# Performance work log

Measured on AMD Instinct MI355X. Metric: run time of the kernel, lower is better.

The kernel has to match this reference:

```python
import jax, jax.numpy as jnp
import numpy as np
from jax import lax

S = 8  # down/up-sample factor


def _seg_means(x, z):
    """Directional running means between zero-boundaries along the last axis.

    x: float [..., L] values; z: bool [..., L], True at zero-boundary positions.
    For position t strictly between consecutive boundaries (prev, nxt):
      lr[t] = mean(x[prev:t+1]),  rl[t] = mean(x[t:nxt+1]); else keep x[t].
    """
    L = x.shape[-1]
    ar = jnp.arange(L)
    ax = x.ndim - 1
    # last zero index strictly before t (-1 if none)
    idx = jnp.where(z, ar, -1)
    prev = lax.cummax(idx, axis=ax)
    prev = jnp.concatenate(
        [jnp.full(prev.shape[:-1] + (1,), -1, prev.dtype), prev[..., :-1]], axis=-1)
    # first zero index strictly after t (L if none)
    idx2 = jnp.where(z, ar, L)
    nxt = lax.cummin(idx2, axis=ax, reverse=True)
    nxt = jnp.concatenate(
        [nxt[..., 1:], jnp.full(nxt.shape[:-1] + (1,), L, nxt.dtype)], axis=-1)
    valid = (~z) & (prev >= 0) & (nxt < L)
    # padded cumsum: cs0[..., k] = sum(x[..., :k]), length L+1
    cs0 = jnp.concatenate(
        [jnp.zeros(x.shape[:-1] + (1,), x.dtype), jnp.cumsum(x, axis=-1)], axis=-1)
    prev_c = jnp.clip(prev, 0, L - 1)
    nxt_c = jnp.clip(nxt, 0, L - 1)
    sum_lr = cs0[..., 1:] - jnp.take_along_axis(cs0, prev_c, axis=-1)   # x[prev..t]
    sum_rl = jnp.take_along_axis(cs0, nxt_c + 1, axis=-1) - cs0[..., :-1]  # x[t..nxt]
    cnt_lr = jnp.maximum(ar - prev + 1, 1).astype(x.dtype)
    cnt_rl = jnp.maximum(nxt - ar + 1, 1).astype(x.dtype)
    lr = jnp.where(valid, sum_lr / cnt_lr, x)
    rl = jnp.where(valid, sum_rl / cnt_rl, x)
    return lr, rl


def setup_inputs() -> dict:
    key = jax.random.key(0)
    k0, k1 = jax.random.split(key)
    N, C, H, W = 8, 1, 2048, 2048
    x0 = jax.random.normal(k0, (N, C, H, W), dtype=jnp.float32)
    x1 = jax.random.randint(k1, (N, C, H, W), 0, 8, dtype=jnp.int32)
    return {"x0": x0, "x1": x1}


def reference(x0, x1):
    # nearest-neighbor downsample by 8 (matches F.interpolate scale_factor=1/8, mode='nearest')
    x0d = x0[..., ::S, ::S]
    zd = (x1[..., ::S, ::S] == 0)
    # horizontal pass (along rows)
    xh_lr, xh_rl = _seg_means(x0d, zd)
    # vertical pass (along columns) via transpose
    xv_tb, xv_bt = _seg_means(jnp.swapaxes(x0d, -1, -2), jnp.swapaxes(zd, -1, -2))
    y = xh_lr + xh_rl + jnp.swapaxes(xv_tb, -1, -2) + jnp.swapaxes(xv_bt, -1, -2)
    # nearest-neighbor upsample by 8
    y = jnp.repeat(jnp.repeat(y, S, axis=-2), S, axis=-1)
    return y
```

## Files before the change

kernel.cpp:

```cpp
#include <hip/hip_runtime.h>

#define DS   256
#define FULL 2048
#define NIMG 8
#define CG   4

typedef float f32x4 __attribute__((ext_vector_type(4)));
typedef int   i32x4 __attribute__((ext_vector_type(4)));

__device__ __forceinline__ float seg_fast(float x, bool z, int j,
                                          float* s_cs,
                                          unsigned long long* s_msk,
                                          float* s_ws) {
    const int lane = j & 63;
    const int w    = j >> 6;
    unsigned long long m = __ballot(z);

    float s = x;
    #pragma unroll
    for (int off = 1; off < 64; off <<= 1) {
        float t = __shfl_up(s, off, 64);
        if (lane >= off) s += t;
    }
    if (lane == 63) s_ws[w]  = s;
    if (lane == 0)  s_msk[w] = m;
    __syncthreads();

    float pre = 0.f;
    for (int ww = 0; ww < w; ++ww) pre += s_ws[ww];
    s += pre;
    s_cs[j] = s;

    unsigned long long lo = m & ((1ULL << lane) - 1ULL);
    int prev = -1;
    if (lo) prev = (w << 6) + 63 - __builtin_clzll(lo);
    else {
        for (int ww = w - 1; ww >= 0; --ww) {
            unsigned long long mm = s_msk[ww];
            if (mm) { prev = (ww << 6) + 63 - __builtin_clzll(mm); break; }
        }
    }
    unsigned long long hi = m & ~((2ULL << lane) - 1ULL);
    int nxt = DS;
    if (hi) nxt = (w << 6) + __builtin_ctzll(hi);
    else {
        for (int ww = w + 1; ww < 4; ++ww) {
            unsigned long long mm = s_msk[ww];
            if (mm) { nxt = (ww << 6) + __builtin_ctzll(mm); break; }
        }
    }
    __syncthreads();

    bool valid = (!z) && (prev >= 0) && (nxt < DS);
    if (valid) {
        float cs_j   = s_cs[j];
        float cs_pm1 = (prev > 0) ? s_cs[prev - 1] : 0.f;
        float cs_n   = s_cs[nxt];
        float cs_jm1 = (j > 0) ? s_cs[j - 1] : 0.f;
        return (cs_j - cs_pm1) / (float)(j - prev + 1)
             + (cs_n - cs_jm1) / (float)(nxt - j + 1);
    }
    return 2.f * x;
}

__global__ __launch_bounds__(256) void k_row(const float* __restrict__ x0,
                                             const int* __restrict__ x1,
                                             float2* __restrict__ xz,
                                             float* __restrict__ yH) {
    __shared__ float s_cs[DS];
    __shared__ unsigned long long s_msk[4];
    __shared__ float s_ws[4];
    const int j = threadIdx.x;
    const int line = blockIdx.x;
    const int n = line >> 8, i = line & 255;

    const float* rb0 = x0 + (size_t)(n * FULL + i * 8) * FULL;
    const int*   rb1 = x1 + (size_t)(n * FULL + i * 8) * FULL;
    f32x4 a = __builtin_nontemporal_load((const f32x4*)(rb0 + 8 * (size_t)j));
    i32x4 b = __builtin_nontemporal_load((const i32x4*)(rb1 + 8 * (size_t)j));
    float x = a[0];
    bool  z = (b[0] == 0);

    float r = seg_fast(x, z, j, s_cs, s_msk, s_ws);

    yH[(line << 8) + j] = r;
    xz[(line << 8) + j] = make_float2(x, z ? 1.f : 0.f);
}

__global__ __launch_bounds__(256) void k_colup(const float2* __restrict__ xz,
                                               const float* __restrict__ yH,
                                               f32x4* __restrict__ out) {
    __shared__ float s_x[CG][DS];
    __shared__ float s_z[CG][DS];
    __shared__ float s_out[CG][DS + 1];
    __shared__ float s_cs[DS];
    __shared__ unsigned long long s_msk[4];
    __shared__ float s_ws[4];
    const int t = threadIdx.x;
    const int g = blockIdx.x;
    const int n  = g >> 7;
    const int q  = (g >> 6) & 1;
    const int c0 = (g & 63) * CG;

    const float2* base = xz + (n << 16) + (t << 8) + c0;
    f32x4 v0 = *(const f32x4*)(base);
    f32x4 v1 = *(const f32x4*)(base + 2);
    f32x4 h  = *(const f32x4*)(yH + (n << 16) + (t << 8) + c0);
    s_x[0][t] = v0[0]; s_z[0][t] = v0[1];
    s_x[1][t] = v0[2]; s_z[1][t] = v0[3];
    s_x[2][t] = v1[0]; s_z[2][t] = v1[1];
    s_x[3][t] = v1[2]; s_z[3][t] = v1[3];

    #pragma unroll
    for (int c = 0; c < CG; ++c) {
        float x = s_x[c][t];
        bool  z = (s_z[c][t] != 0.f);
        float r = seg_fast(x, z, t, s_cs, s_msk, s_ws);
        s_out[c][t] = r + h[c];
    }
    __syncthreads();

    f32x4* ob = out + ((size_t)n << 20) + (c0 << 1);
    #pragma unroll 4
    for (int k = 0; k < 16; ++k) {
        int idx = (k << 8) + t;
        int I   = (q << 10) + (idx >> 2);
        int c   = idx & 3;
        float v = s_out[c][I >> 3];
        f32x4 vv = { v, v, v, v };
        size_t o = (size_t)I * 512 + (c << 1);
        ob[o]     = vv;
        ob[o + 1] = vv;
    }
}

extern "C" void kernel_launch(void* const* d_in, const int* in_sizes, int n_in,
                              void* d_out, int out_size, void* d_ws, size_t ws_size,
                              hipStream_t stream) {
    const float* x0 = (const float*)d_in[0];
    const int*   x1 = (const int*)d_in[1];
    f32x4* out = (f32x4*)d_out;

    float2* xz = (float2*)d_ws;
    float*  yH = (float*)(xz + NIMG * DS * DS);

    dim3 blk(256);
    k_row  <<<dim3(NIMG * DS),          blk, 0, stream>>>(x0, x1, xz, yH);
    k_colup<<<dim3(2 * NIMG * DS / CG), blk, 0, stream>>>(xz, yH, out);
}
```

Measured before the change: 43.46 us.

## Widen column-group tile to eight columns and quarter output rows per block

The column/upsample kernel now processes eight downsampled columns per block instead of four, and splits the output rows into four quarters instead of two. Each upsampled row segment written per block becomes twice as wide, so output stores are more contiguous. Column inputs now stay in registers instead of going through shared-memory staging. In exchange, each column's segment scan is recomputed by four blocks instead of two, and each block runs eight sync-heavy scans in sequence.

```diff
diff --git a/kernel.cpp b/kernel.cpp
--- a/kernel.cpp
+++ b/kernel.cpp
@@ -3,7 +3,7 @@
 #define DS   256
 #define FULL 2048
 #define NIMG 8
-#define CG   4
+#define CG   8
 
 typedef float f32x4 __attribute__((ext_vector_type(4)));
 typedef int   i32x4 __attribute__((ext_vector_type(4)));
@@ -90,8 +90,6 @@
 __global__ __launch_bounds__(256) void k_colup(const float2* __restrict__ xz,
                                                const float* __restrict__ yH,
                                                f32x4* __restrict__ out) {
-    __shared__ float s_x[CG][DS];
-    __shared__ float s_z[CG][DS];
     __shared__ float s_out[CG][DS + 1];
     __shared__ float s_cs[DS];
     __shared__ unsigned long long s_msk[4];
@@ -99,36 +97,38 @@
     const int t = threadIdx.x;
     const int g = blockIdx.x;
     const int n  = g >> 7;
-    const int q  = (g >> 6) & 1;
-    const int c0 = (g & 63) * CG;
+    const int q  = (g >> 5) & 3;
+    const int c0 = (g & 31) << 3;
 
     const float2* base = xz + (n << 16) + (t << 8) + c0;
     f32x4 v0 = *(const f32x4*)(base);
     f32x4 v1 = *(const f32x4*)(base + 2);
-    f32x4 h  = *(const f32x4*)(yH + (n << 16) + (t << 8) + c0);
-    s_x[0][t] = v0[0]; s_z[0][t] = v0[1];
-    s_x[1][t] = v0[2]; s_z[1][t] = v0[3];
-    s_x[2][t] = v1[0]; s_z[2][t] = v1[1];
-    s_x[3][t] = v1[2]; s_z[3][t] = v1[3];
+    f32x4 v2 = *(const f32x4*)(base + 4);
+    f32x4 v3 = *(const f32x4*)(base + 6);
+    const float* hb = yH + (n << 16) + (t << 8) + c0;
+    f32x4 h0 = *(const f32x4*)(hb);
+    f32x4 h1 = *(const f32x4*)(hb + 4);
+
+    float xa[CG] = { v0[0], v0[2], v1[0], v1[2], v2[0], v2[2], v3[0], v3[2] };
+    float za[CG] = { v0[1], v0[3], v1[1], v1[3], v2[1], v2[3], v3[1], v3[3] };
+    float ha[CG] = { h0[0], h0[1], h0[2], h0[3], h1[0], h1[1], h1[2], h1[3] };
 
     #pragma unroll
     for (int c = 0; c < CG; ++c) {
-        float x = s_x[c][t];
-        bool  z = (s_z[c][t] != 0.f);
-        float r = seg_fast(x, z, t, s_cs, s_msk, s_ws);
-        s_out[c][t] = r + h[c];
+        float r = seg_fast(xa[c], za[c] != 0.f, t, s_cs, s_msk, s_ws);
+        s_out[c][t] = r + ha[c];
     }
     __syncthreads();
 
-    f32x4* ob = out + ((size_t)n << 20) + (c0 << 1);
-    #pragma unroll 4
+    f32x4* ob = out + ((size_t)n << 20);
+    #pragma unroll
     for (int k = 0; k < 16; ++k) {
         int idx = (k << 8) + t;
-        int I   = (q << 10) + (idx >> 2);
-        int c   = idx & 3;
-        float v = s_out[c][I >> 3];
+        int I   = (q << 9) + (idx >> 3);
+        int p   = idx & 7;
+        float v = s_out[p][I >> 3];
         f32x4 vv = { v, v, v, v };
-        size_t o = (size_t)I * 512 + (c << 1);
+        size_t o = (size_t)I * 512 + ((c0 + p) << 1);
         ob[o]     = vv;
         ob[o + 1] = vv;
     }
@@ -145,6 +145,6 @@
     float*  yH = (float*)(xz + NIMG * DS * DS);
 
     dim3 blk(256);
-    k_row  <<<dim3(NIMG * DS),          blk, 0, stream>>>(x0, x1, xz, yH);
-    k_colup<<<dim3(2 * NIMG * DS / CG), blk, 0, stream>>>(xz, yH, out);
+    k_row  <<<dim3(NIMG * DS),              blk, 0, stream>>>(x0, x1, xz, yH);
+    k_colup<<<dim3(NIMG * (DS / CG) * 4),   blk, 0, stream>>>(xz, yH, out);
 }
```

Result: slower. 45.15 us (+3.9%).
